# Performance work log

Measured on AMD Instinct MI355X. Metric: run time of the kernel, lower is better.

## Reference

```python
import jax, jax.numpy as jnp
import numpy as np

C = 256       # in_channels
A = 6         # act_dim
B = 10000     # number of graphs (batch)
N = B * A     # total nodes
E = 960000    # number of edges
H = 32        # hidden_size


def setup_inputs() -> dict:
    key = jax.random.key(0)
    ks = jax.random.split(key, 20)
    s = 1.0 / np.sqrt(C)
    inp = {
        "state": jax.random.normal(ks[0], (N, C), jnp.float32),
        "edge_index": jax.random.randint(ks[1], (2, E), 0, N, jnp.int32),
        "action": jax.random.uniform(ks[2], (B, A), jnp.float32),
    }
    # GCNConv params (weight [C,C], bias [C]); conv4/conv5 exist but are unused by forward
    for i in range(5):
        inp[f"W{i+1}"] = jax.random.normal(ks[3 + i], (C, C), jnp.float32) * s
        inp[f"b{i+1}"] = jnp.zeros((C,), jnp.float32)
    D1 = 6 * C + 1
    inp["lin1_w"] = jax.random.normal(ks[10], (D1, H), jnp.float32) / np.sqrt(D1)
    inp["lin1_b"] = jnp.zeros((H,), jnp.float32)
    inp["lin2_w"] = jax.random.normal(ks[11], (H, H), jnp.float32) / np.sqrt(H)
    inp["lin2_b"] = jnp.zeros((H,), jnp.float32)
    inp["lin3_w"] = jax.random.normal(ks[12], (H, 1), jnp.float32) / np.sqrt(H)
    inp["lin3_b"] = jnp.zeros((1,), jnp.float32)
    return inp


def _gcn(x, W, b, src, dst, dinv):
    # PyG GCNConv: xW, then D^{-1/2}(A+I)D^{-1/2} aggregation, then bias.
    xw = x @ W                                    # [N, C]
    norm = dinv[src] * dinv[dst]                  # [E]
    agg = jax.ops.segment_sum(xw[src] * norm[:, None], dst, num_segments=N)
    agg = agg + xw * (dinv * dinv)[:, None]       # self-loop term
    return agg + b


def reference(state, edge_index, action,
              W1, b1, W2, b2, W3, b3, W4, b4, W5, b5,
              lin1_w, lin1_b, lin2_w, lin2_b, lin3_w, lin3_b):
    src, dst = edge_index[0], edge_index[1]
    # degree of A + I, computed at destination nodes (gcn_norm with self-loops)
    deg = jax.ops.segment_sum(jnp.ones((E,), state.dtype), dst, num_segments=N) + 1.0
    dinv = jax.lax.rsqrt(deg)

    o1 = jax.nn.relu(_gcn(state, W1, b1, src, dst, dinv))
    o2 = jax.nn.relu(_gcn(o1, W2, b2, src, dst, dinv))
    o3 = jax.nn.relu(_gcn(o2, W3, b3, src, dst, dinv))
    # NOTE: original forward reuses conv3 for layers 4 and 5 (replicated faithfully)
    o4 = jax.nn.relu(_gcn(o3, W3, b3, src, dst, dinv))
    o5 = jax.nn.relu(_gcn(o4, W3, b3, src, dst, dinv))

    r = lambda t: t.reshape(-1, A, C)             # [B, A, C]
    concat = jnp.concatenate(
        [r(o1), r(o2), r(o3), r(o4), r(o5), r(state), action[..., None]], axis=-1)
    x = jax.nn.relu(concat @ lin1_w + lin1_b)     # [B, A, H]
    x = jax.nn.relu(x @ lin2_w + lin2_b)
    x = jnp.sum(x, axis=1)                        # readout over act_dim
    x = (x @ lin3_w + lin3_b).squeeze(-1)         # [B]
    return x
```

## Files before the change

### kernel.cpp

```cpp
#include <hip/hip_runtime.h>
#include <hip/hip_fp16.h>

#define NNODES 60000
#define NEDGES 960000
#define NGRAPH 10000

struct __align__(16) H8 { __half2 h[4]; };
struct __align__(8)  H4 { __half2 h[2]; };

typedef _Float16 f16x8 __attribute__((ext_vector_type(8)));
typedef float f32x4 __attribute__((ext_vector_type(4)));

#define LDA 264


__global__ void count_deg_k(const int* __restrict__ ei, int* __restrict__ deg) {
  int e = blockIdx.x * blockDim.x + threadIdx.x;
  atomicAdd(&deg[ei[NEDGES + e]], 1);
}

__global__ void scan1_k(const int* __restrict__ deg, int* __restrict__ rs,
                        int* __restrict__ bsum, float* __restrict__ dinv) {
  __shared__ int s[256];
  int tid = threadIdx.x;
  int i = blockIdx.x * 256 + tid;
  int v = (i < NNODES) ? deg[i] : 0;
  if (i < NNODES) dinv[i] = rsqrtf((float)v + 1.0f);
  int x = v;
  s[tid] = x; __syncthreads();
  #pragma unroll
  for (int off = 1; off < 256; off <<= 1) {
    int t = (tid >= off) ? s[tid - off] : 0;
    __syncthreads();
    x += t; s[tid] = x; __syncthreads();
  }
  if (i < NNODES) rs[i] = x - v;
  if (tid == 255) bsum[blockIdx.x] = x;
}

__global__ void scan2_k(int* __restrict__ bsum, int nb) {
  __shared__ int s[256];
  int tid = threadIdx.x;
  int v = (tid < nb) ? bsum[tid] : 0;
  int x = v; s[tid] = x; __syncthreads();
  #pragma unroll
  for (int off = 1; off < 256; off <<= 1) {
    int t = (tid >= off) ? s[tid - off] : 0;
    __syncthreads();
    x += t; s[tid] = x; __syncthreads();
  }
  if (tid < nb) bsum[tid] = x - v;
}

__global__ void scan3_k(int* __restrict__ rs, const int* __restrict__ bsum) {
  int i = blockIdx.x * 256 + threadIdx.x;
  if (i < NNODES) rs[i] += bsum[blockIdx.x];
  if (i == 0) rs[NNODES] = NEDGES;
}

__global__ void scatter_k(const int* __restrict__ ei, const int* __restrict__ rs,
                          int* __restrict__ cursor, unsigned short* __restrict__ csr) {
  int e = blockIdx.x * blockDim.x + threadIdx.x;
  int s = ei[e], d = ei[NEDGES + e];
  int pos = rs[d] + atomicAdd(&cursor[d], 1);
  csr[pos] = (unsigned short)s;
}


__global__ void prep_k(const float* __restrict__ W1, const float* __restrict__ W2,
                       const float* __restrict__ W3, const float* __restrict__ l1w,
                       __half* __restrict__ B1, __half* __restrict__ B2,
                       __half* __restrict__ B3, __half* __restrict__ Pp,
                       int* __restrict__ deg, int* __restrict__ cursor) {
  int bid = blockIdx.x;
  int t = threadIdx.x;
  if (bid < 384) {
    int which = bid >> 7;
    int c = bid & 127;
    const float* W = which == 0 ? W1 : (which == 1 ? W2 : W3);
    __half* Bp = which == 0 ? B1 : (which == 1 ? B2 : B3);
    int kq = c >> 4, wcf = c & 15;
    int l = t >> 2;
    int j0 = (t & 3) * 2;
    int li = l & 15, lg = l >> 4;
    int n = wcf * 16 + li;
    int k = kq * 32 + lg * 8 + j0;
    __half2 v;
    v.x = __float2half_rn(W[(size_t)k * 256 + n]);
    v.y = __float2half_rn(W[(size_t)(k + 1) * 256 + n]);
    *reinterpret_cast<__half2*>(Bp + (size_t)c * 512 + 2 * t) = v;
  } else {
    int b = bid - 384;
    int l = b >> 4, cp = b & 15;
    int kq = cp >> 1, hh = cp & 1;
    int ln = t >> 2;
    int j0 = (t & 3) * 2;
    int li = ln & 15, lg = ln >> 4;
    int dim = hh * 16 + li;
    int k = kq * 32 + lg * 8 + j0;
    __half2 v;
    v.x = __float2half_rn(l1w[((size_t)l * 256 + k) * 32 + dim]);
    v.y = __float2half_rn(l1w[((size_t)l * 256 + k + 1) * 32 + dim]);
    *reinterpret_cast<__half2*>(Pp + (size_t)b * 512 + 2 * t) = v;
  }
  int z = bid * 256 + t;
  if (z < NNODES) deg[z] = 0;
  else if (z < 2 * NNODES) cursor[z - NNODES] = 0;
}


__device__ __forceinline__ void gemm_body256(
    _Float16 (*As)[LDA], int m0, int tid,
    const __half* __restrict__ Bp, const __half* __restrict__ Pp,
    const float* __restrict__ dinv, __half* __restrict__ Y,
    float* __restrict__ part) {
  const int lane = tid & 63;
  const int wid = tid >> 6;
  const int wr2 = wid >> 1, wcl = wid & 1;
  const int li = lane & 15, lg = lane >> 4;

  f32x4 acc[8];
  #pragma unroll
  for (int j = 0; j < 8; ++j) acc[j] = (f32x4){0.f, 0.f, 0.f, 0.f};
  f32x4 p = (f32x4){0.f, 0.f, 0.f, 0.f};

  const __half* bwave = Bp + (size_t)(wcl * 8) * 512 + lane * 8;
  const __half* pbase = Pp + (size_t)wcl * 512 + lane * 8;

  #pragma unroll
  for (int kq = 0; kq < 8; ++kq) {
    f16x8 a = *reinterpret_cast<const f16x8*>(&As[wr2 * 16 + li][kq * 32 + lg * 8]);
    {
      f16x8 b0 = *reinterpret_cast<const f16x8*>(bwave + ((size_t)kq * 16 + 0) * 512);
      f16x8 b1 = *reinterpret_cast<const f16x8*>(bwave + ((size_t)kq * 16 + 1) * 512);
      f16x8 b2 = *reinterpret_cast<const f16x8*>(bwave + ((size_t)kq * 16 + 2) * 512);
      f16x8 b3 = *reinterpret_cast<const f16x8*>(bwave + ((size_t)kq * 16 + 3) * 512);
      acc[0] = __builtin_amdgcn_mfma_f32_16x16x32_f16(b0, a, acc[0], 0, 0, 0);
      acc[1] = __builtin_amdgcn_mfma_f32_16x16x32_f16(b1, a, acc[1], 0, 0, 0);
      acc[2] = __builtin_amdgcn_mfma_f32_16x16x32_f16(b2, a, acc[2], 0, 0, 0);
      acc[3] = __builtin_amdgcn_mfma_f32_16x16x32_f16(b3, a, acc[3], 0, 0, 0);
    }
    {
      f16x8 b4 = *reinterpret_cast<const f16x8*>(bwave + ((size_t)kq * 16 + 4) * 512);
      f16x8 b5 = *reinterpret_cast<const f16x8*>(bwave + ((size_t)kq * 16 + 5) * 512);
      f16x8 b6 = *reinterpret_cast<const f16x8*>(bwave + ((size_t)kq * 16 + 6) * 512);
      f16x8 b7 = *reinterpret_cast<const f16x8*>(bwave + ((size_t)kq * 16 + 7) * 512);
      acc[4] = __builtin_amdgcn_mfma_f32_16x16x32_f16(b4, a, acc[4], 0, 0, 0);
      acc[5] = __builtin_amdgcn_mfma_f32_16x16x32_f16(b5, a, acc[5], 0, 0, 0);
      acc[6] = __builtin_amdgcn_mfma_f32_16x16x32_f16(b6, a, acc[6], 0, 0, 0);
      acc[7] = __builtin_amdgcn_mfma_f32_16x16x32_f16(b7, a, acc[7], 0, 0, 0);
    }
    {
      f16x8 bp = *reinterpret_cast<const f16x8*>(pbase + (size_t)kq * 2 * 512);
      p = __builtin_amdgcn_mfma_f32_16x16x32_f16(bp, a, p, 0, 0, 0);
    }
  }

  __syncthreads();

  {
    int row = wr2 * 16 + li;
    int r = m0 + row;
    float dv = dinv[r];
    #pragma unroll
    for (int cf = 0; cf < 8; ++cf) {
      int col = wcl * 128 + cf * 16 + lg * 4;
      H4 o;
      o.h[0].x = __float2half_rn(acc[cf][0] * dv);
      o.h[0].y = __float2half_rn(acc[cf][1] * dv);
      o.h[1].x = __float2half_rn(acc[cf][2] * dv);
      o.h[1].y = __float2half_rn(acc[cf][3] * dv);
      *reinterpret_cast<H4*>(&As[row][col]) = o;
    }
    float4 v;
    v.x = p[0]; v.y = p[1]; v.z = p[2]; v.w = p[3];
    *reinterpret_cast<float4*>(part + (size_t)r * 32 + wcl * 16 + lg * 4) = v;
  }

  __syncthreads();

  #pragma unroll
  for (int l = 0; l < 4; ++l) {
    int f = l * 256 + tid;
    int row = f >> 5, c8 = (f & 31) * 8;
    *reinterpret_cast<H8*>(Y + (size_t)(m0 + row) * 256 + c8) =
        *reinterpret_cast<const H8*>(&As[row][c8]);
  }
}


__launch_bounds__(256, 5)
__global__ void gemm0_k(const float* __restrict__ Xf, const __half* __restrict__ Bp,
                        const float* __restrict__ dinv, __half* __restrict__ Y,
                        const __half* __restrict__ Pp, float* __restrict__ part) {
  __shared__ _Float16 As[32][LDA];
  const int tid = threadIdx.x;
  const int m0 = blockIdx.x * 32;
  #pragma unroll
  for (int l = 0; l < 4; ++l) {
    int f = l * 256 + tid;
    int row = f >> 5, c8 = (f & 31) * 8;
    const float* src = Xf + (size_t)(m0 + row) * 256 + c8;
    float4 u = *reinterpret_cast<const float4*>(src);
    float4 v = *reinterpret_cast<const float4*>(src + 4);
    H8 o;
    o.h[0].x = __float2half_rn(u.x); o.h[0].y = __float2half_rn(u.y);
    o.h[1].x = __float2half_rn(u.z); o.h[1].y = __float2half_rn(u.w);
    o.h[2].x = __float2half_rn(v.x); o.h[2].y = __float2half_rn(v.y);
    o.h[3].x = __float2half_rn(v.z); o.h[3].y = __float2half_rn(v.w);
    *reinterpret_cast<H8*>(&As[row][c8]) = o;
  }
  __syncthreads();
  gemm_body256(As, m0, tid, Bp, Pp, dinv, Y, part);
}


__launch_bounds__(256, 5)
__global__ void gemm_k(const __half* __restrict__ Xh, const __half* __restrict__ Bp,
                       const float* __restrict__ dinv, __half* __restrict__ Y,
                       const __half* __restrict__ Pp, float* __restrict__ part) {
  __shared__ _Float16 As[32][LDA];
  const int tid = threadIdx.x;
  const int m0 = blockIdx.x * 32;
  #pragma unroll
  for (int l = 0; l < 4; ++l) {
    int f = l * 256 + tid;
    int row = f >> 5, c8 = (f & 31) * 8;
    *reinterpret_cast<H8*>(&As[row][c8]) =
        *reinterpret_cast<const H8*>(Xh + (size_t)(m0 + row) * 256 + c8);
  }
  __syncthreads();
  gemm_body256(As, m0, tid, Bp, Pp, dinv, Y, part);
}


__launch_bounds__(256, 4)
__global__ void proj_k(const __half* __restrict__ Xh, const __half* __restrict__ Pp,
                       float* __restrict__ part) {
  __shared__ _Float16 As[64][LDA];
  const int tid = threadIdx.x;
  const int m0 = blockIdx.x * 64;
  #pragma unroll
  for (int l = 0; l < 8; ++l) {
    int f = l * 256 + tid;
    int row = f >> 5, c8 = (f & 31) * 8;
    *reinterpret_cast<H8*>(&As[row][c8]) =
        *reinterpret_cast<const H8*>(Xh + (size_t)(m0 + row) * 256 + c8);
  }
  __syncthreads();

  const int lane = tid & 63;
  const int wid = tid >> 6;
  const int li = lane & 15, lg = lane >> 4;
  const __half* pbase = Pp + lane * 8;

  f32x4 p0 = (f32x4){0.f, 0.f, 0.f, 0.f};
  f32x4 p1 = (f32x4){0.f, 0.f, 0.f, 0.f};
  #pragma unroll
  for (int kq = 0; kq < 8; ++kq) {
    int k0 = kq * 32;
    f16x8 ap = *reinterpret_cast<const f16x8*>(&As[wid * 16 + li][k0 + lg * 8]);
    f16x8 bp0 = *reinterpret_cast<const f16x8*>(pbase + ((size_t)kq * 2 + 0) * 512);
    f16x8 bp1 = *reinterpret_cast<const f16x8*>(pbase + ((size_t)kq * 2 + 1) * 512);
    p0 = __builtin_amdgcn_mfma_f32_16x16x32_f16(bp0, ap, p0, 0, 0, 0);
    p1 = __builtin_amdgcn_mfma_f32_16x16x32_f16(bp1, ap, p1, 0, 0, 0);
  }
  int pr = m0 + wid * 16 + li;
  {
    float4 v0, v1;
    v0.x = p0[0]; v0.y = p0[1]; v0.z = p0[2]; v0.w = p0[3];
    v1.x = p1[0]; v1.y = p1[1]; v1.z = p1[2]; v1.w = p1[3];
    *reinterpret_cast<float4*>(part + (size_t)pr * 32 + lg * 4) = v0;
    *reinterpret_cast<float4*>(part + (size_t)pr * 32 + 16 + lg * 4) = v1;
  }
}


__device__ inline void addH8(float* acc, const H8& v) {
  #pragma unroll
  for (int q = 0; q < 4; ++q) {
    acc[q * 2 + 0] += __low2float(v.h[q]);
    acc[q * 2 + 1] += __high2float(v.h[q]);
  }
}

__global__ void gather_k(const __half* __restrict__ ysh, const int* __restrict__ rs,
                         const unsigned short* __restrict__ csr, const float* __restrict__ dinv,
                         const float* __restrict__ bias, __half* __restrict__ out) {
  int tid = threadIdx.x;
  int lane = tid & 63;
  int wave = (blockIdx.x * blockDim.x + tid) >> 6;
  int d = wave * 2 + (lane >> 5);
  int c8 = (lane & 31) * 8;

  float acc[8];
  H8 self = *reinterpret_cast<const H8*>(ysh + (size_t)d * 256 + c8);
  #pragma unroll
  for (int q = 0; q < 4; ++q) {
    acc[q * 2 + 0] = __low2float(self.h[q]);
    acc[q * 2 + 1] = __high2float(self.h[q]);
  }

  int e = rs[d], end = rs[d + 1];
  for (; e + 3 < end; e += 4) {
    int s0 = csr[e], s1 = csr[e + 1], s2 = csr[e + 2], s3 = csr[e + 3];
    H8 v0 = *reinterpret_cast<const H8*>(ysh + (size_t)s0 * 256 + c8);
    H8 v1 = *reinterpret_cast<const H8*>(ysh + (size_t)s1 * 256 + c8);
    H8 v2 = *reinterpret_cast<const H8*>(ysh + (size_t)s2 * 256 + c8);
    H8 v3 = *reinterpret_cast<const H8*>(ysh + (size_t)s3 * 256 + c8);
    addH8(acc, v0);
    addH8(acc, v1);
    addH8(acc, v2);
    addH8(acc, v3);
  }
  for (; e < end; ++e) {
    int s0 = csr[e];
    H8 v0 = *reinterpret_cast<const H8*>(ysh + (size_t)s0 * 256 + c8);
    addH8(acc, v0);
  }

  float dv = dinv[d];
  float4 b0 = *reinterpret_cast<const float4*>(bias + c8);
  float4 b1 = *reinterpret_cast<const float4*>(bias + c8 + 4);
  float r0 = fmaxf(acc[0] * dv + b0.x, 0.f);
  float r1 = fmaxf(acc[1] * dv + b0.y, 0.f);
  float r2 = fmaxf(acc[2] * dv + b0.z, 0.f);
  float r3 = fmaxf(acc[3] * dv + b0.w, 0.f);
  float r4 = fmaxf(acc[4] * dv + b1.x, 0.f);
  float r5 = fmaxf(acc[5] * dv + b1.y, 0.f);
  float r6 = fmaxf(acc[6] * dv + b1.z, 0.f);
  float r7 = fmaxf(acc[7] * dv + b1.w, 0.f);
  H8 o;
  o.h[0].x = __float2half_rn(r0); o.h[0].y = __float2half_rn(r1);
  o.h[1].x = __float2half_rn(r2); o.h[1].y = __float2half_rn(r3);
  o.h[2].x = __float2half_rn(r4); o.h[2].y = __float2half_rn(r5);
  o.h[3].x = __float2half_rn(r6); o.h[3].y = __float2half_rn(r7);
  *reinterpret_cast<H8*>(out + (size_t)d * 256 + c8) = o;
}


__launch_bounds__(192)
__global__ void mlpfinal_k(const float* __restrict__ p0, const float* __restrict__ p1,
                           const float* __restrict__ p2, const float* __restrict__ p3,
                           const float* __restrict__ p4, const float* __restrict__ p5,
                           const float* __restrict__ action, const float* __restrict__ l1wlast,
                           const float* __restrict__ l1b, const float* __restrict__ l2w,
                           const float* __restrict__ l2b, const float* __restrict__ l3w,
                           const float* __restrict__ l3b, float* __restrict__ out) {
  __shared__ float w2s[1024];
  __shared__ float h1s[6][33];
  __shared__ float red[3];
  int tid = threadIdx.x;
  for (int i = tid; i < 1024; i += 192) w2s[i] = l2w[i];
  int a = tid >> 5, dim = tid & 31;
  int n = blockIdx.x * 6 + a;
  int idx = n * 32 + dim;
  float h1 = l1b[dim] + action[n] * l1wlast[dim]
           + p0[idx] + p1[idx] + p2[idx] + p3[idx] + p4[idx] + p5[idx];
  h1s[a][dim] = fmaxf(h1, 0.f);
  __syncthreads();
  float acc = l2b[dim];
  #pragma unroll
  for (int k = 0; k < 32; ++k) acc += h1s[a][k] * w2s[k * 32 + dim];
  float v = fmaxf(acc, 0.f) * l3w[dim];
  #pragma unroll
  for (int off = 32; off; off >>= 1) v += __shfl_down(v, off, 64);
  int lane = tid & 63, wave = tid >> 6;
  if (lane == 0) red[wave] = v;
  __syncthreads();
  if (tid == 0) out[blockIdx.x] = red[0] + red[1] + red[2] + l3b[0];
}


extern "C" void kernel_launch(void* const* d_in, const int* in_sizes, int n_in,
                              void* d_out, int out_size, void* d_ws, size_t ws_size,
                              hipStream_t stream) {
  const float* state  = (const float*)d_in[0];
  const int*   ei     = (const int*)d_in[1];
  const float* action = (const float*)d_in[2];
  const float* W1 = (const float*)d_in[3];
  const float* b1 = (const float*)d_in[4];
  const float* W2 = (const float*)d_in[5];
  const float* b2 = (const float*)d_in[6];
  const float* W3 = (const float*)d_in[7];
  const float* b3 = (const float*)d_in[8];
  const float* l1w = (const float*)d_in[13];
  const float* l1b = (const float*)d_in[14];
  const float* l2w = (const float*)d_in[15];
  const float* l2b = (const float*)d_in[16];
  const float* l3w = (const float*)d_in[17];
  const float* l3b = (const float*)d_in[18];
  float* out = (float*)d_out;

  char* base = (char*)d_ws;
  size_t off = 0;
  auto carve = [&](size_t bytes) {
    char* q = base + off;
    off += (bytes + 255) & ~(size_t)255;
    return q;
  };
  __half* ysh   = (__half*)carve((size_t)NNODES * 256 * 2);
  __half* obufh = (__half*)carve((size_t)NNODES * 256 * 2);
  __half* Bp1   = (__half*)carve(128 * 512 * 2);
  __half* Bp2   = (__half*)carve(128 * 512 * 2);
  __half* Bp3   = (__half*)carve(128 * 512 * 2);
  __half* Pp    = (__half*)carve(96 * 512 * 2);
  float* parts[6];
  for (int i = 0; i < 6; ++i) parts[i] = (float*)carve((size_t)NNODES * 32 * 4);
  float* dinv  = (float*)carve(NNODES * 4);
  int*   deg   = (int*)carve(NNODES * 4);
  int*   cursor= (int*)carve(NNODES * 4);
  int*   rs    = (int*)carve((NNODES + 1) * 4);
  unsigned short* csr = (unsigned short*)carve((size_t)NEDGES * 2);
  int*   bsum  = (int*)carve(256 * 4);

  prep_k<<<480, 256, 0, stream>>>(W1, W2, W3, l1w, Bp1, Bp2, Bp3, Pp, deg, cursor);

  count_deg_k<<<NEDGES / 256, 256, 0, stream>>>(ei, deg);
  int nb = (NNODES + 255) / 256;
  scan1_k<<<nb, 256, 0, stream>>>(deg, rs, bsum, dinv);
  scan2_k<<<1, 256, 0, stream>>>(bsum, nb);
  scan3_k<<<nb, 256, 0, stream>>>(rs, bsum);
  scatter_k<<<NEDGES / 256, 256, 0, stream>>>(ei, rs, cursor, csr);

  int gblocks = NNODES / 32;
  const __half* Bps[5] = {Bp1, Bp2, Bp3, Bp3, Bp3};
  const float*  bs[5]  = {b1, b2, b3, b3, b3};

  gemm0_k<<<gblocks, 256, 0, stream>>>(state, Bp1, dinv, ysh,
                                       Pp + (size_t)5 * 16 * 512, parts[5]);
  for (int layer = 1; layer < 5; ++layer) {
    gather_k<<<NNODES / 8, 256, 0, stream>>>(ysh, rs, csr, dinv, bs[layer - 1], obufh);
    gemm_k<<<gblocks, 256, 0, stream>>>(obufh, Bps[layer], dinv, ysh,
                                        Pp + (size_t)(layer - 1) * 16 * 512, parts[layer - 1]);
  }
  gather_k<<<NNODES / 8, 256, 0, stream>>>(ysh, rs, csr, dinv, b3, obufh);
  proj_k<<<NNODES / 64, 256, 0, stream>>>(obufh, Pp + (size_t)4 * 16 * 512, parts[4]);

  mlpfinal_k<<<NGRAPH, 192, 0, stream>>>(parts[0], parts[1], parts[2], parts[3], parts[4],
                                         parts[5], action, l1w + 1536 * 32, l1b, l2w, l2b,
                                         l3w, l3b, out);
}
```

Baseline: 618.7 us.

## Write gather output in MFMA fragment layout and load A directly from global

The gather kernel now stores its output in a layout pre-swizzled for the MFMA A-operand, 16-row tiles split into k-quarter fragments. gemm_k and proj_k load A fragments straight from global memory with no LDS staging or block barrier. gemm_k now assigns each wave a 16-row by 128-column output tile instead of a block-wide 32-row tile, with a small per-wave LDS buffer to coalesce stores. Each A fragment is now read by two waves, and each wave issues more B loads from global.

```diff
diff --git a/kernel.cpp b/kernel.cpp
--- a/kernel.cpp
+++ b/kernel.cpp
@@ -188,7 +188,6 @@
   }
 }
 
-
 __launch_bounds__(256, 5)
 __global__ void gemm0_k(const float* __restrict__ Xf, const __half* __restrict__ Bp,
                         const float* __restrict__ dinv, __half* __restrict__ Y,
@@ -215,64 +214,110 @@
 }
 
 
-__launch_bounds__(256, 5)
-__global__ void gemm_k(const __half* __restrict__ Xh, const __half* __restrict__ Bp,
+__launch_bounds__(256, 6)
+__global__ void gemm_k(const __half* __restrict__ Xp, const __half* __restrict__ Bp,
                        const float* __restrict__ dinv, __half* __restrict__ Y,
                        const __half* __restrict__ Pp, float* __restrict__ part) {
-  __shared__ _Float16 As[32][LDA];
+  __shared__ _Float16 osw[4][16][136];
   const int tid = threadIdx.x;
-  const int m0 = blockIdx.x * 32;
-  #pragma unroll
-  for (int l = 0; l < 4; ++l) {
-    int f = l * 256 + tid;
-    int row = f >> 5, c8 = (f & 31) * 8;
-    *reinterpret_cast<H8*>(&As[row][c8]) =
-        *reinterpret_cast<const H8*>(Xh + (size_t)(m0 + row) * 256 + c8);
-  }
-  __syncthreads();
-  gemm_body256(As, m0, tid, Bp, Pp, dinv, Y, part);
-}
-
-
-__launch_bounds__(256, 4)
-__global__ void proj_k(const __half* __restrict__ Xh, const __half* __restrict__ Pp,
-                       float* __restrict__ part) {
-  __shared__ _Float16 As[64][LDA];
-  const int tid = threadIdx.x;
-  const int m0 = blockIdx.x * 64;
-  #pragma unroll
-  for (int l = 0; l < 8; ++l) {
-    int f = l * 256 + tid;
-    int row = f >> 5, c8 = (f & 31) * 8;
-    *reinterpret_cast<H8*>(&As[row][c8]) =
-        *reinterpret_cast<const H8*>(Xh + (size_t)(m0 + row) * 256 + c8);
-  }
-  __syncthreads();
-
   const int lane = tid & 63;
   const int wid = tid >> 6;
+  const int gw = blockIdx.x * 4 + wid;
+  const int t = gw >> 1, wcl = gw & 1;
   const int li = lane & 15, lg = lane >> 4;
+
+  f32x4 acc[8];
+  #pragma unroll
+  for (int j = 0; j < 8; ++j) acc[j] = (f32x4){0.f, 0.f, 0.f, 0.f};
+  f32x4 p = (f32x4){0.f, 0.f, 0.f, 0.f};
+
+  const __half* abase = Xp + (size_t)t * 4096 + lane * 8;
+  const __half* bwave = Bp + (size_t)(wcl * 8) * 512 + lane * 8;
+  const __half* pbase = Pp + (size_t)wcl * 512 + lane * 8;
+
+  #pragma unroll
+  for (int kq = 0; kq < 8; ++kq) {
+    f16x8 a = *reinterpret_cast<const f16x8*>(abase + (size_t)kq * 512);
+    {
+      f16x8 b0 = *reinterpret_cast<const f16x8*>(bwave + ((size_t)kq * 16 + 0) * 512);
+      f16x8 b1 = *reinterpret_cast<const f16x8*>(bwave + ((size_t)kq * 16 + 1) * 512);
+      f16x8 b2 = *reinterpret_cast<const f16x8*>(bwave + ((size_t)kq * 16 + 2) * 512);
+      f16x8 b3 = *reinterpret_cast<const f16x8*>(bwave + ((size_t)kq * 16 + 3) * 512);
+      acc[0] = __builtin_amdgcn_mfma_f32_16x16x32_f16(b0, a, acc[0], 0, 0, 0);
+      acc[1] = __builtin_amdgcn_mfma_f32_16x16x32_f16(b1, a, acc[1], 0, 0, 0);
+      acc[2] = __builtin_amdgcn_mfma_f32_16x16x32_f16(b2, a, acc[2], 0, 0, 0);
+      acc[3] = __builtin_amdgcn_mfma_f32_16x16x32_f16(b3, a, acc[3], 0, 0, 0);
+    }
+    {
+      f16x8 b4 = *reinterpret_cast<const f16x8*>(bwave + ((size_t)kq * 16 + 4) * 512);
+      f16x8 b5 = *reinterpret_cast<const f16x8*>(bwave + ((size_t)kq * 16 + 5) * 512);
+      f16x8 b6 = *reinterpret_cast<const f16x8*>(bwave + ((size_t)kq * 16 + 6) * 512);
+      f16x8 b7 = *reinterpret_cast<const f16x8*>(bwave + ((size_t)kq * 16 + 7) * 512);
+      acc[4] = __builtin_amdgcn_mfma_f32_16x16x32_f16(b4, a, acc[4], 0, 0, 0);
+      acc[5] = __builtin_amdgcn_mfma_f32_16x16x32_f16(b5, a, acc[5], 0, 0, 0);
+      acc[6] = __builtin_amdgcn_mfma_f32_16x16x32_f16(b6, a, acc[6], 0, 0, 0);
+      acc[7] = __builtin_amdgcn_mfma_f32_16x16x32_f16(b7, a, acc[7], 0, 0, 0);
+    }
+    {
+      f16x8 bp = *reinterpret_cast<const f16x8*>(pbase + (size_t)kq * 2 * 512);
+      p = __builtin_amdgcn_mfma_f32_16x16x32_f16(bp, a, p, 0, 0, 0);
+    }
+  }
+
+  int r = t * 16 + li;
+  float dv = dinv[r];
+  #pragma unroll
+  for (int cf = 0; cf < 8; ++cf) {
+    H4 o;
+    o.h[0].x = __float2half_rn(acc[cf][0] * dv);
+    o.h[0].y = __float2half_rn(acc[cf][1] * dv);
+    o.h[1].x = __float2half_rn(acc[cf][2] * dv);
+    o.h[1].y = __float2half_rn(acc[cf][3] * dv);
+    *reinterpret_cast<H4*>(&osw[wid][li][cf * 16 + lg * 4]) = o;
+  }
+  {
+    float4 v;
+    v.x = p[0]; v.y = p[1]; v.z = p[2]; v.w = p[3];
+    *reinterpret_cast<float4*>(part + (size_t)r * 32 + wcl * 16 + lg * 4) = v;
+  }
+  #pragma unroll
+  for (int l = 0; l < 4; ++l) {
+    int idx = l * 64 + lane;
+    int row = idx >> 4, c8 = (idx & 15) * 8;
+    *reinterpret_cast<H8*>(Y + (size_t)(t * 16 + row) * 256 + wcl * 128 + c8) =
+        *reinterpret_cast<const H8*>(&osw[wid][row][c8]);
+  }
+}
+
+
+__launch_bounds__(256, 8)
+__global__ void proj_k(const __half* __restrict__ Xp, const __half* __restrict__ Pp,
+                       float* __restrict__ part) {
+  const int tid = threadIdx.x;
+  const int lane = tid & 63;
+  const int wid = tid >> 6;
+  const int t = blockIdx.x * 4 + wid;
+  if (t >= NNODES / 16) return;
+  const int li = lane & 15, lg = lane >> 4;
+  const __half* abase = Xp + (size_t)t * 4096 + lane * 8;
   const __half* pbase = Pp + lane * 8;
 
   f32x4 p0 = (f32x4){0.f, 0.f, 0.f, 0.f};
   f32x4 p1 = (f32x4){0.f, 0.f, 0.f, 0.f};
   #pragma unroll
   for (int kq = 0; kq < 8; ++kq) {
-    int k0 = kq * 32;
-    f16x8 ap = *reinterpret_cast<const f16x8*>(&As[wid * 16 + li][k0 + lg * 8]);
+    f16x8 a = *reinterpret_cast<const f16x8*>(abase + (size_t)kq * 512);
     f16x8 bp0 = *reinterpret_cast<const f16x8*>(pbase + ((size_t)kq * 2 + 0) * 512);
     f16x8 bp1 = *reinterpret_cast<const f16x8*>(pbase + ((size_t)kq * 2 + 1) * 512);
-    p0 = __builtin_amdgcn_mfma_f32_16x16x32_f16(bp0, ap, p0, 0, 0, 0);
-    p1 = __builtin_amdgcn_mfma_f32_16x16x32_f16(bp1, ap, p1, 0, 0, 0);
-  }
-  int pr = m0 + wid * 16 + li;
-  {
-    float4 v0, v1;
-    v0.x = p0[0]; v0.y = p0[1]; v0.z = p0[2]; v0.w = p0[3];
-    v1.x = p1[0]; v1.y = p1[1]; v1.z = p1[2]; v1.w = p1[3];
-    *reinterpret_cast<float4*>(part + (size_t)pr * 32 + lg * 4) = v0;
-    *reinterpret_cast<float4*>(part + (size_t)pr * 32 + 16 + lg * 4) = v1;
-  }
+    p0 = __builtin_amdgcn_mfma_f32_16x16x32_f16(bp0, a, p0, 0, 0, 0);
+    p1 = __builtin_amdgcn_mfma_f32_16x16x32_f16(bp1, a, p1, 0, 0, 0);
+  }
+  int r = t * 16 + li;
+  float4 v0, v1;
+  v0.x = p0[0]; v0.y = p0[1]; v0.z = p0[2]; v0.w = p0[3];
+  v1.x = p1[0]; v1.y = p1[1]; v1.z = p1[2]; v1.w = p1[3];
+  *reinterpret_cast<float4*>(part + (size_t)r * 32 + lg * 4) = v0;
+  *reinterpret_cast<float4*>(part + (size_t)r * 32 + 16 + lg * 4) = v1;
 }
 
 
@@ -335,7 +380,10 @@
   o.h[1].x = __float2half_rn(r2); o.h[1].y = __float2half_rn(r3);
   o.h[2].x = __float2half_rn(r4); o.h[2].y = __float2half_rn(r5);
   o.h[3].x = __float2half_rn(r6); o.h[3].y = __float2half_rn(r7);
-  *reinterpret_cast<H8*>(out + (size_t)d * 256 + c8) = o;
+
+  int t = d >> 4, pli = d & 15;
+  int kq = c8 >> 5, plg = (c8 >> 3) & 3;
+  *reinterpret_cast<H8*>(out + (size_t)t * 4096 + (size_t)kq * 512 + (plg * 16 + pli) * 8) = o;
 }
 
 
@@ -423,19 +471,18 @@
   scan3_k<<<nb, 256, 0, stream>>>(rs, bsum);
   scatter_k<<<NEDGES / 256, 256, 0, stream>>>(ei, rs, cursor, csr);
 
-  int gblocks = NNODES / 32;
   const __half* Bps[5] = {Bp1, Bp2, Bp3, Bp3, Bp3};
   const float*  bs[5]  = {b1, b2, b3, b3, b3};
 
-  gemm0_k<<<gblocks, 256, 0, stream>>>(state, Bp1, dinv, ysh,
-                                       Pp + (size_t)5 * 16 * 512, parts[5]);
+  gemm0_k<<<NNODES / 32, 256, 0, stream>>>(state, Bp1, dinv, ysh,
+                                           Pp + (size_t)5 * 16 * 512, parts[5]);
   for (int layer = 1; layer < 5; ++layer) {
     gather_k<<<NNODES / 8, 256, 0, stream>>>(ysh, rs, csr, dinv, bs[layer - 1], obufh);
-    gemm_k<<<gblocks, 256, 0, stream>>>(obufh, Bps[layer], dinv, ysh,
-                                        Pp + (size_t)(layer - 1) * 16 * 512, parts[layer - 1]);
+    gemm_k<<<(NNODES / 16) * 2 / 4, 256, 0, stream>>>(obufh, Bps[layer], dinv, ysh,
+        Pp + (size_t)(layer - 1) * 16 * 512, parts[layer - 1]);
   }
   gather_k<<<NNODES / 8, 256, 0, stream>>>(ysh, rs, csr, dinv, b3, obufh);
-  proj_k<<<NNODES / 64, 256, 0, stream>>>(obufh, Pp + (size_t)4 * 16 * 512, parts[4]);
+  proj_k<<<(NNODES / 16 + 3) / 4, 256, 0, stream>>>(obufh, Pp + (size_t)4 * 16 * 512, parts[4]);
 
   mlpfinal_k<<<NGRAPH, 192, 0, stream>>>(parts[0], parts[1], parts[2], parts[3], parts[4],
                                          parts[5], action, l1w + 1536 * 32, l1b, l2w, l2b,
```

Measured after the change: 622.7 us. About the same (+0.7%).
